# Performance work log

Hardware: AMD Instinct MI355X
Metric: run time of the kernel (lower is better)

The kernel has to match this reference:

```python
import jax, jax.numpy as jnp
import numpy as np

B, H, S, DK = 2, 16, 2048, 64
NEG = jnp.float32(-10000.0)


def setup_inputs() -> dict:
    key = jax.random.key(0)
    kq, kk, kv, km = jax.random.split(key, 4)
    query = jax.random.normal(kq, (B, H, S, DK), dtype=jnp.float32)
    k_ = jax.random.normal(kk, (B, H, S, DK), dtype=jnp.float32)
    value = jax.random.normal(kv, (B, H, S, DK), dtype=jnp.float32)
    mask = (jax.random.uniform(km, (B, 1, S, S)) > 0.5).astype(jnp.float32)
    return {"query": query, "key": k_, "value": value, "mask": mask, "d_k": DK}


def reference(query, key, value, mask, d_k):
    # scores: [B,H,S,S]
    scale = jnp.float32(1.0 / np.sqrt(d_k))
    scores = jnp.einsum('bhqd,bhkd->bhqk', query, key) * scale * mask
    # non-standard masking: keep only strictly positive masked scores
    scores = jnp.where(scores > 0, scores, NEG)
    attn = jax.nn.softmax(scores, axis=-1)
    return jnp.einsum('bhqk,bhkd->bhqd', attn, value)
```

## Files before the change

### kernel.cpp

```cpp
#include <hip/hip_runtime.h>
#include <hip/hip_bf16.h>
#include <math.h>

#define S_LEN 2048
#define D_KV  64
#define BQ    128
#define BK    64
#define LP    72
#define NW    8

typedef __attribute__((ext_vector_type(8))) short bh8;
typedef __attribute__((ext_vector_type(4))) short sh4;
typedef __attribute__((ext_vector_type(4))) float fx4;

__device__ __forceinline__ short f2bf(float f) {
    unsigned u = __builtin_bit_cast(unsigned, f);
    u += 0x7fffu + ((u >> 16) & 1u);
    return (short)(u >> 16);
}

__global__ __launch_bounds__(512, 4)
void attn_fwd(const float* __restrict__ Qg, const float* __restrict__ Kg,
              const float* __restrict__ Vg, const float* __restrict__ Mg,
              float* __restrict__ Og)
{
    __shared__ __align__(16) short k_lds[BK * LP];
    __shared__ __align__(16) short v_lds[D_KV * LP];
    __shared__ __align__(16) short p_lds[NW * 16 * LP];

    const int tid  = threadIdx.x;
    const int wave = tid >> 6;
    const int lane = tid & 63;
    const int g    = lane >> 4;
    const int c    = lane & 15;

    const int qt = blockIdx.x;
    const int bh = blockIdx.y;
    const int b  = bh >> 4;

    const int qw = qt * BQ + wave * 16;

    const float* Qp = Qg + ((size_t)bh * S_LEN + qw) * D_KV;
    const float* Kp = Kg + (size_t)bh * S_LEN * D_KV;
    const float* Vp = Vg + (size_t)bh * S_LEN * D_KV;
    const float* Mp = Mg + (size_t)b * S_LEN * S_LEN;
    float*       Op = Og + ((size_t)bh * S_LEN + qw) * D_KV;

    bh8 qf[2];
#pragma unroll
    for (int kc = 0; kc < 2; ++kc) {
        const float* src = Qp + c * D_KV + kc * 32 + g * 8;
        float4 a0 = *(const float4*)(src);
        float4 a1 = *(const float4*)(src + 4);
        bh8 f;
        f[0] = f2bf(a0.x * 0.125f); f[1] = f2bf(a0.y * 0.125f);
        f[2] = f2bf(a0.z * 0.125f); f[3] = f2bf(a0.w * 0.125f);
        f[4] = f2bf(a1.x * 0.125f); f[5] = f2bf(a1.y * 0.125f);
        f[6] = f2bf(a1.z * 0.125f); f[7] = f2bf(a1.w * 0.125f);
        qf[kc] = f;
    }

    fx4 o[4];
    float l_r[4];
#pragma unroll
    for (int u = 0; u < 4; ++u) { fx4 z = {0.f, 0.f, 0.f, 0.f}; o[u] = z; }
#pragma unroll
    for (int r = 0; r < 4; ++r) l_r[r] = 0.f;

    for (int kt = 0; kt < S_LEN; kt += BK) {
#pragma unroll
        for (int i = 0; i < 2; ++i) {
            int idx = tid + 512 * i;
            int kr  = idx >> 4;
            int db  = (idx & 15) * 4;
            float4 kv = *(const float4*)(Kp + (size_t)(kt + kr) * D_KV + db);
            sh4 s4;
            s4[0] = f2bf(kv.x); s4[1] = f2bf(kv.y);
            s4[2] = f2bf(kv.z); s4[3] = f2bf(kv.w);
            *(sh4*)&k_lds[kr * LP + db] = s4;
        }
        {
            int kr = lane;
#pragma unroll
            for (int i = 0; i < 2; ++i) {
                int db = wave * 8 + i * 4;
                float4 vv = *(const float4*)(Vp + (size_t)(kt + kr) * D_KV + db);
                v_lds[(db + 0) * LP + kr] = f2bf(vv.x);
                v_lds[(db + 1) * LP + kr] = f2bf(vv.y);
                v_lds[(db + 2) * LP + kr] = f2bf(vv.z);
                v_lds[(db + 3) * LP + kr] = f2bf(vv.w);
            }
        }
        __syncthreads();

        fx4 sacc[4];
#pragma unroll
        for (int t = 0; t < 4; ++t) { fx4 z = {0.f, 0.f, 0.f, 0.f}; sacc[t] = z; }
#pragma unroll
        for (int kc = 0; kc < 2; ++kc) {
#pragma unroll
            for (int t = 0; t < 4; ++t) {
                bh8 kf = *(const bh8*)&k_lds[(t * 16 + c) * LP + kc * 32 + g * 8];
                sacc[t] = __builtin_amdgcn_mfma_f32_16x16x32_bf16(qf[kc], kf, sacc[t], 0, 0, 0);
            }
        }

        const float* mbase = Mp + (size_t)(qw + g * 4) * S_LEN + kt + c;
        float mv[4][4];
#pragma unroll
        for (int t = 0; t < 4; ++t)
#pragma unroll
            for (int r = 0; r < 4; ++r)
                mv[t][r] = mbase[(size_t)r * S_LEN + t * 16];

        short* pw = &p_lds[wave * 16 * LP];
#pragma unroll
        for (int t = 0; t < 4; ++t)
#pragma unroll
            for (int r = 0; r < 4; ++r) {
                float tm = sacc[t][r] * mv[t][r];
                float p  = (tm > 0.f) ? __expf(tm) : 0.f;
                l_r[r] += p;
                pw[(g * 4 + r) * LP + t * 16 + c] = f2bf(p);
            }

#pragma unroll
        for (int kc = 0; kc < 2; ++kc) {
            bh8 pa = *(const bh8*)&pw[c * LP + kc * 32 + g * 8];
#pragma unroll
            for (int u = 0; u < 4; ++u) {
                bh8 vb = *(const bh8*)&v_lds[(u * 16 + c) * LP + kc * 32 + g * 8];
                o[u] = __builtin_amdgcn_mfma_f32_16x16x32_bf16(pa, vb, o[u], 0, 0, 0);
            }
        }
        __syncthreads();
    }

#pragma unroll
    for (int r = 0; r < 4; ++r) {
#pragma unroll
        for (int off = 8; off >= 1; off >>= 1)
            l_r[r] += __shfl_xor(l_r[r], off, 16);
    }

#pragma unroll
    for (int r = 0; r < 4; ++r) {
        float inv = 1.0f / l_r[r];
#pragma unroll
        for (int u = 0; u < 4; ++u)
            Op[(size_t)(g * 4 + r) * D_KV + u * 16 + c] = o[u][r] * inv;
    }
}

extern "C" void kernel_launch(void* const* d_in, const int* in_sizes, int n_in,
                              void* d_out, int out_size, void* d_ws, size_t ws_size,
                              hipStream_t stream) {
    const float* Q = (const float*)d_in[0];
    const float* K = (const float*)d_in[1];
    const float* V = (const float*)d_in[2];
    const float* M = (const float*)d_in[3];
    float*       O = (float*)d_out;
    dim3 grid(S_LEN / BQ, 32);
    attn_fwd<<<grid, 512, 0, stream>>>(Q, K, V, M, O);
}
```

Before: 188.4 us.

## Switch attention to 32x32x16 MFMA tiles with 4 waves of 32 query rows

Replaces the 16x16x32 bf16 MFMA tiling with 32x32x16 MFMA, so each wave now owns 32 query rows and the block drops from 8 waves to 4 (256 threads). Larger MFMA tiles cut the number of LDS fragment loads per flop, since each K and V fragment feeds a bigger output tile. Each thread now holds more accumulator registers (two 16-wide accumulators for S and O plus 16 row sums). Fewer waves per block and lower occupancy could reduce latency hiding for the global mask and K/V loads.

```diff
diff --git a/kernel.cpp b/kernel.cpp
--- a/kernel.cpp
+++ b/kernel.cpp
@@ -7,11 +7,11 @@
 #define BQ    128
 #define BK    64
 #define LP    72
-#define NW    8
+#define NW    4
 
-typedef __attribute__((ext_vector_type(8))) short bh8;
-typedef __attribute__((ext_vector_type(4))) short sh4;
-typedef __attribute__((ext_vector_type(4))) float fx4;
+typedef __attribute__((ext_vector_type(8)))  short bh8;
+typedef __attribute__((ext_vector_type(4)))  short sh4;
+typedef __attribute__((ext_vector_type(16))) float f32x16;
 
 __device__ __forceinline__ short f2bf(float f) {
     unsigned u = __builtin_bit_cast(unsigned, f);
@@ -19,26 +19,26 @@
     return (short)(u >> 16);
 }
 
-__global__ __launch_bounds__(512, 4)
+__global__ __launch_bounds__(256, 2)
 void attn_fwd(const float* __restrict__ Qg, const float* __restrict__ Kg,
               const float* __restrict__ Vg, const float* __restrict__ Mg,
               float* __restrict__ Og)
 {
     __shared__ __align__(16) short k_lds[BK * LP];
     __shared__ __align__(16) short v_lds[D_KV * LP];
-    __shared__ __align__(16) short p_lds[NW * 16 * LP];
+    __shared__ __align__(16) short p_lds[NW * 32 * LP];
 
     const int tid  = threadIdx.x;
     const int wave = tid >> 6;
     const int lane = tid & 63;
-    const int g    = lane >> 4;
-    const int c    = lane & 15;
+    const int n    = lane & 31;
+    const int hi   = lane >> 5;
 
     const int qt = blockIdx.x;
     const int bh = blockIdx.y;
     const int b  = bh >> 4;
 
-    const int qw = qt * BQ + wave * 16;
+    const int qw = qt * BQ + wave * 32;
 
     const float* Qp = Qg + ((size_t)bh * S_LEN + qw) * D_KV;
     const float* Kp = Kg + (size_t)bh * S_LEN * D_KV;
@@ -46,10 +46,10 @@
     const float* Mp = Mg + (size_t)b * S_LEN * S_LEN;
     float*       Op = Og + ((size_t)bh * S_LEN + qw) * D_KV;
 
-    bh8 qf[2];
+    bh8 qf[4];
 #pragma unroll
-    for (int kc = 0; kc < 2; ++kc) {
-        const float* src = Qp + c * D_KV + kc * 32 + g * 8;
+    for (int kc = 0; kc < 4; ++kc) {
+        const float* src = Qp + n * D_KV + kc * 16 + hi * 8;
         float4 a0 = *(const float4*)(src);
         float4 a1 = *(const float4*)(src + 4);
         bh8 f;
@@ -60,17 +60,15 @@
         qf[kc] = f;
     }
 
-    fx4 o[4];
-    float l_r[4];
+    f32x16 o0, o1;
+    float  l_r[16];
 #pragma unroll
-    for (int u = 0; u < 4; ++u) { fx4 z = {0.f, 0.f, 0.f, 0.f}; o[u] = z; }
-#pragma unroll
-    for (int r = 0; r < 4; ++r) l_r[r] = 0.f;
+    for (int i = 0; i < 16; ++i) { o0[i] = 0.f; o1[i] = 0.f; l_r[i] = 0.f; }
 
     for (int kt = 0; kt < S_LEN; kt += BK) {
 #pragma unroll
-        for (int i = 0; i < 2; ++i) {
-            int idx = tid + 512 * i;
+        for (int i = 0; i < 4; ++i) {
+            int idx = tid + 256 * i;
             int kr  = idx >> 4;
             int db  = (idx & 15) * 4;
             float4 kv = *(const float4*)(Kp + (size_t)(kt + kr) * D_KV + db);
@@ -82,8 +80,8 @@
         {
             int kr = lane;
 #pragma unroll
-            for (int i = 0; i < 2; ++i) {
-                int db = wave * 8 + i * 4;
+            for (int i = 0; i < 4; ++i) {
+                int db = wave * 16 + i * 4;
                 float4 vv = *(const float4*)(Vp + (size_t)(kt + kr) * D_KV + db);
                 v_lds[(db + 0) * LP + kr] = f2bf(vv.x);
                 v_lds[(db + 1) * LP + kr] = f2bf(vv.y);
@@ -93,62 +91,61 @@
         }
         __syncthreads();
 
-        fx4 sacc[4];
+        f32x16 s0, s1;
 #pragma unroll
-        for (int t = 0; t < 4; ++t) { fx4 z = {0.f, 0.f, 0.f, 0.f}; sacc[t] = z; }
+        for (int i = 0; i < 16; ++i) { s0[i] = 0.f; s1[i] = 0.f; }
 #pragma unroll
-        for (int kc = 0; kc < 2; ++kc) {
-#pragma unroll
-            for (int t = 0; t < 4; ++t) {
-                bh8 kf = *(const bh8*)&k_lds[(t * 16 + c) * LP + kc * 32 + g * 8];
-                sacc[t] = __builtin_amdgcn_mfma_f32_16x16x32_bf16(qf[kc], kf, sacc[t], 0, 0, 0);
-            }
+        for (int kc = 0; kc < 4; ++kc) {
+            int off = kc * 16 + hi * 8;
+            bh8 b0 = *(const bh8*)&k_lds[n * LP + off];
+            bh8 b1 = *(const bh8*)&k_lds[(32 + n) * LP + off];
+            s0 = __builtin_amdgcn_mfma_f32_32x32x16_bf16(qf[kc], b0, s0, 0, 0, 0);
+            s1 = __builtin_amdgcn_mfma_f32_32x32x16_bf16(qf[kc], b1, s1, 0, 0, 0);
         }
 
-        const float* mbase = Mp + (size_t)(qw + g * 4) * S_LEN + kt + c;
-        float mv[4][4];
+        short* pw = &p_lds[wave * 32 * LP];
+        const float* mb = Mp + (size_t)(qw + 4 * hi) * S_LEN + kt + n;
 #pragma unroll
-        for (int t = 0; t < 4; ++t)
-#pragma unroll
-            for (int r = 0; r < 4; ++r)
-                mv[t][r] = mbase[(size_t)r * S_LEN + t * 16];
-
-        short* pw = &p_lds[wave * 16 * LP];
-#pragma unroll
-        for (int t = 0; t < 4; ++t)
-#pragma unroll
-            for (int r = 0; r < 4; ++r) {
-                float tm = sacc[t][r] * mv[t][r];
-                float p  = (tm > 0.f) ? __expf(tm) : 0.f;
-                l_r[r] += p;
-                pw[(g * 4 + r) * LP + t * 16 + c] = f2bf(p);
-            }
+        for (int r = 0; r < 16; ++r) {
+            int rowo = (r & 3) + 8 * (r >> 2);
+            const float* mrow = mb + (size_t)rowo * S_LEN;
+            float m0 = mrow[0];
+            float m1 = mrow[32];
+            float t0 = s0[r] * m0;
+            float t1 = s1[r] * m1;
+            float p0 = (t0 > 0.f) ? __expf(t0) : 0.f;
+            float p1 = (t1 > 0.f) ? __expf(t1) : 0.f;
+            l_r[r] += p0 + p1;
+            int prow = (rowo + 4 * hi) * LP;
+            pw[prow + n]      = f2bf(p0);
+            pw[prow + 32 + n] = f2bf(p1);
+        }
 
 #pragma unroll
-        for (int kc = 0; kc < 2; ++kc) {
-            bh8 pa = *(const bh8*)&pw[c * LP + kc * 32 + g * 8];
-#pragma unroll
-            for (int u = 0; u < 4; ++u) {
-                bh8 vb = *(const bh8*)&v_lds[(u * 16 + c) * LP + kc * 32 + g * 8];
-                o[u] = __builtin_amdgcn_mfma_f32_16x16x32_bf16(pa, vb, o[u], 0, 0, 0);
-            }
+        for (int kc = 0; kc < 4; ++kc) {
+            int off = kc * 16 + hi * 8;
+            bh8 pa = *(const bh8*)&pw[n * LP + off];
+            bh8 v0 = *(const bh8*)&v_lds[n * LP + off];
+            bh8 v1 = *(const bh8*)&v_lds[(32 + n) * LP + off];
+            o0 = __builtin_amdgcn_mfma_f32_32x32x16_bf16(pa, v0, o0, 0, 0, 0);
+            o1 = __builtin_amdgcn_mfma_f32_32x32x16_bf16(pa, v1, o1, 0, 0, 0);
         }
         __syncthreads();
     }
 
 #pragma unroll
-    for (int r = 0; r < 4; ++r) {
+    for (int r = 0; r < 16; ++r) {
 #pragma unroll
-        for (int off = 8; off >= 1; off >>= 1)
-            l_r[r] += __shfl_xor(l_r[r], off, 16);
+        for (int off = 16; off >= 1; off >>= 1)
+            l_r[r] += __shfl_xor(l_r[r], off, 32);
     }
 
 #pragma unroll
-    for (int r = 0; r < 4; ++r) {
+    for (int r = 0; r < 16; ++r) {
+        int qrow = (r & 3) + 8 * (r >> 2) + 4 * hi;
         float inv = 1.0f / l_r[r];
-#pragma unroll
-        for (int u = 0; u < 4; ++u)
-            Op[(size_t)(g * 4 + r) * D_KV + u * 16 + c] = o[u][r] * inv;
+        Op[(size_t)qrow * D_KV + n]      = o0[r] * inv;
+        Op[(size_t)qrow * D_KV + 32 + n] = o1[r] * inv;
     }
 }
 
@@ -161,5 +158,5 @@
     const float* M = (const float*)d_in[3];
     float*       O = (float*)d_out;
     dim3 grid(S_LEN / BQ, 32);
-    attn_fwd<<<grid, 512, 0, stream>>>(Q, K, V, M, O);
+    attn_fwd<<<grid, 256, 0, stream>>>(Q, K, V, M, O);
 }
```

Result: slower. 229.3 us (+21.7%).
